# Kernel tuning notes

Hardware: AMD Instinct MI355X
Metric: run time of the kernel (lower is better)

Reference implementation:

```python
import jax, jax.numpy as jnp
import numpy as np

# Config constants (from DeepSeekConfig / init_kwargs)
NUM_EXPERTS = 6
VAR_EXPERTS = 4
FIXED_EXPERTS = NUM_EXPERTS - VAR_EXPERTS  # 2
TOP_K = 2
D_MODEL = 1024
D_FF = 4 * D_MODEL
LN_EPS = 1e-5


def setup_inputs() -> dict:
    key = jax.random.key(0)
    ks = jax.random.split(key, 6)
    B, S = 2, 2048
    x = jax.random.normal(ks[0], (B, S, D_MODEL), dtype=jnp.float32)
    router_W = jax.random.normal(ks[1], (D_MODEL, VAR_EXPERTS), dtype=jnp.float32) * 0.02
    # stacked expert FFN params: (E, D, 4D) and (E, 4D, D)
    W1 = jax.random.normal(ks[2], (NUM_EXPERTS, D_MODEL, D_FF), dtype=jnp.float32) * 0.02
    b1 = jnp.zeros((NUM_EXPERTS, D_FF), dtype=jnp.float32)
    W2 = jax.random.normal(ks[3], (NUM_EXPERTS, D_FF, D_MODEL), dtype=jnp.float32) * 0.02
    b2 = jnp.zeros((NUM_EXPERTS, D_MODEL), dtype=jnp.float32)
    ln_gamma = jnp.ones((D_MODEL,), dtype=jnp.float32)
    ln_beta = jnp.zeros((D_MODEL,), dtype=jnp.float32)
    return {"x": x, "router_W": router_W, "W1": W1, "b1": b1, "W2": W2,
            "b2": b2, "ln_gamma": ln_gamma, "ln_beta": ln_beta}


def reference(x, router_W, W1, b1, W2, b2, ln_gamma, ln_beta):
    B, S, D = x.shape
    # router over the VARIABLE experts only
    router_logits = jnp.einsum('bsd,de->bse', x, router_W)          # (B,S,VAR)
    router_probs = jax.nn.softmax(router_logits, axis=-1)
    _, topk_idx = jax.lax.top_k(router_probs, TOP_K)                 # (B,S,K)
    adj_idx = topk_idx + FIXED_EXPERTS                               # global expert ids in [FIXED, NUM)

    # dense per-expert FFN on all tokens: experts[e](x) = gelu(x@W1[e]+b1[e]) @ W2[e] + b2[e]
    h = jnp.einsum('bsd,edf->ebsf', x, W1) + b1[:, None, None, :]    # (E,B,S,4D)
    h = jax.nn.gelu(h, approximate=False)                            # torch F.gelu default = exact
    all_out = jnp.einsum('ebsf,efd->ebsd', h, W2) + b2[:, None, None, :]  # (E,B,S,D)

    # fixed experts: all of experts[0:FIXED] applied to every token
    fixed_sum = all_out[:FIXED_EXPERTS].sum(axis=0)                  # (B,S,D)

    # variable experts: per-token gather of the top-k selected experts
    b_ix = jnp.arange(B)[:, None, None]
    s_ix = jnp.arange(S)[None, :, None]
    var = all_out[adj_idx, b_ix, s_ix, :]                            # (B,S,K,D)

    # cat along expert slot dim then mean == sum / (FIXED + K); topk probs unused (plain mean)
    combined = (fixed_sum + var.sum(axis=2)) / (FIXED_EXPERTS + TOP_K)

    # LayerNorm (biased variance, eps=1e-5)
    mu = combined.mean(axis=-1, keepdims=True)
    v = combined.var(axis=-1, keepdims=True)
    out = (combined - mu) / jnp.sqrt(v + LN_EPS) * ln_gamma + ln_beta
    return out, router_logits
```

## Files before the change

### kernel.cpp

```cpp
#include <hip/hip_runtime.h>
#include <cstdint>
#include <cstddef>

#define D_MODEL 1024
#define D_FF 4096
#define NTOK 4096
#define LN_EPS 1e-5f
#define SLAB_ROWS 17408

typedef __bf16 bf16x8 __attribute__((ext_vector_type(8)));
typedef float f32x4 __attribute__((ext_vector_type(4)));
typedef unsigned short u16x4 __attribute__((ext_vector_type(4)));
typedef unsigned short u16x8 __attribute__((ext_vector_type(8)));

static __device__ __forceinline__ unsigned short f2bf(float f) {
    union { float f; unsigned u; } v; v.f = f;
    unsigned r = v.u + 0x7fffu + ((v.u >> 16) & 1u);
    return (unsigned short)(r >> 16);
}

static __device__ __forceinline__ float b2f(unsigned short u) {
    union { unsigned u; float f; } v; v.u = (unsigned)u << 16;
    return v.f;
}

static __device__ __forceinline__ float gelu_fast(float x) {
    float x2 = x * x;
    float a = x * __builtin_fmaf(-0.0713548162726f, x2, -1.59576912161f);
    float e = __expf(a);
    return x * __builtin_amdgcn_rcpf(1.0f + e);
}

static __device__ __forceinline__ void gload16(const void* g, void* l) {
    __builtin_amdgcn_global_load_lds(
        (const __attribute__((address_space(1))) void*)g,
        (__attribute__((address_space(3))) void*)l, 16, 0, 0);
}

static __device__ __forceinline__ void seg_of(const int* cnt, int seg[4], int pc[4]) {
    int o = 2 * NTOK;
    #pragma unroll
    for (int e = 0; e < 4; ++e) {
        int c = cnt[e * 32];
        pc[e] = (c + 255) & ~255;
        seg[e] = o;
        o += pc[e];
    }
}

__global__ __launch_bounds__(256) void convx_kernel(const float* __restrict__ x,
                                                    unsigned short* __restrict__ xb) {
    int idx = blockIdx.x * 256 + threadIdx.x;
    f32x4 v = *(const f32x4*)&x[(size_t)idx * 4];
    u16x4 b;
    b[0] = f2bf(v[0]); b[1] = f2bf(v[1]); b[2] = f2bf(v[2]); b[3] = f2bf(v[3]);
    *(u16x4*)&xb[(size_t)idx * 4] = b;
}

__global__ __launch_bounds__(256) void transpose_kernel(const float* __restrict__ W,
                                                        unsigned short* __restrict__ Wt,
                                                        int K, int N) {
    __shared__ unsigned short t[64][65];
    int k0 = blockIdx.y * 64, n0 = blockIdx.x * 64;
    const float* We = W + (size_t)blockIdx.z * K * N;
    unsigned short* Wte = Wt + (size_t)blockIdx.z * K * N;
    #pragma unroll
    for (int i = 0; i < 4; ++i) {
        int idx = threadIdx.x + i * 256;
        int kr = idx >> 4, c4 = idx & 15;
        f32x4 v = *(const f32x4*)&We[(size_t)(k0 + kr) * N + n0 + c4 * 4];
        #pragma unroll
        for (int j = 0; j < 4; ++j) t[c4 * 4 + j][kr] = f2bf(v[j]);
    }
    __syncthreads();
    #pragma unroll
    for (int i = 0; i < 2; ++i) {
        int idx = threadIdx.x + i * 256;
        int nr = idx >> 3, ck = idx & 7;
        u16x8 w;
        #pragma unroll
        for (int j = 0; j < 8; ++j) w[j] = t[nr][ck * 8 + j];
        *(u16x8*)&Wte[(size_t)(n0 + nr) * K + k0 + ck * 8] = w;
    }
}

__global__ __launch_bounds__(256) void router_kernel(
        const float* __restrict__ x, const float* __restrict__ rW,
        float* __restrict__ logits, int* __restrict__ selpk,
        int* __restrict__ slotpk, int* __restrict__ cnt, int* __restrict__ list) {
    __shared__ int se[8];
    __shared__ int sslot[8];
    int wid = threadIdx.x >> 6, lane = threadIdx.x & 63;
    int t = blockIdx.x * 4 + wid;
    const float* xr = x + (size_t)t * D_MODEL;
    float a0 = 0.f, a1 = 0.f, a2 = 0.f, a3 = 0.f;
    for (int d = lane; d < D_MODEL; d += 64) {
        float xv = xr[d];
        const float* w = rW + d * 4;
        a0 += xv * w[0]; a1 += xv * w[1]; a2 += xv * w[2]; a3 += xv * w[3];
    }
    #pragma unroll
    for (int off = 32; off; off >>= 1) {
        a0 += __shfl_xor(a0, off); a1 += __shfl_xor(a1, off);
        a2 += __shfl_xor(a2, off); a3 += __shfl_xor(a3, off);
    }
    if (lane == 0) {
        float l[4] = {a0, a1, a2, a3};
        logits[t * 4 + 0] = a0; logits[t * 4 + 1] = a1;
        logits[t * 4 + 2] = a2; logits[t * 4 + 3] = a3;
        int e0 = 0; float b = l[0];
        #pragma unroll
        for (int e = 1; e < 4; ++e) if (l[e] > b) { b = l[e]; e0 = e; }
        int e1 = -1; float b2 = -1e30f;
        #pragma unroll
        for (int e = 0; e < 4; ++e) {
            if (e == e0) continue;
            if (l[e] > b2) { b2 = l[e]; e1 = e; }
        }
        se[wid * 2] = e0; se[wid * 2 + 1] = e1;
    }
    __syncthreads();
    if (threadIdx.x == 0) {
        int cnts[4] = {0, 0, 0, 0}, base[4];
        #pragma unroll
        for (int k = 0; k < 8; ++k) cnts[se[k]]++;
        #pragma unroll
        for (int e = 0; e < 4; ++e)
            if (cnts[e]) base[e] = atomicAdd(&cnt[e * 32], cnts[e]);
        int run[4] = {0, 0, 0, 0};
        #pragma unroll
        for (int k = 0; k < 8; ++k) {
            int e = se[k];
            int s = base[e] + run[e]++;
            sslot[k] = s;
            list[e * NTOK + s] = blockIdx.x * 4 + (k >> 1);
        }
    }
    __syncthreads();
    if (lane == 0) {
        selpk[t] = se[wid * 2] | (se[wid * 2 + 1] << 8);
        slotpk[t] = sslot[wid * 2] | (sslot[wid * 2 + 1] << 16);
    }
}

template<int GELU>
__global__ __launch_bounds__(512, 2) void gemm8_kernel(
        const unsigned short* __restrict__ A, const unsigned short* __restrict__ B,
        const float* __restrict__ bias, int bias_stride, int ldo,
        unsigned short* __restrict__ out,
        const int* __restrict__ cnt, const int* __restrict__ list, int K) {
    __shared__ unsigned short lds[2][2][256 * 64];
    const int e = blockIdx.z;
    const int tid = threadIdx.x, l = tid & 63, w = tid >> 6;
    int rowbase;
    int ecnt = NTOK;
    if (e < 2) {
        rowbase = e * NTOK + blockIdx.y * 256;
    } else {
        int seg[4], pc[4];
        seg_of(cnt, seg, pc);
        int ev = e - 2;
        ecnt = cnt[ev * 32];
        if ((int)blockIdx.y * 256 >= pc[ev]) return;
        rowbase = seg[ev] + blockIdx.y * 256;
    }
    const int n0 = blockIdx.x * 256;
    const unsigned short* Be = B + (size_t)e * (4096 * 1024);

    const unsigned short* asrc[4];
    const unsigned short* bsrc[4];
    #pragma unroll
    for (int i = 0; i < 4; ++i) {
        int row = i * 64 + w * 8 + (l >> 3);
        int piece = ((l & 7) ^ (row & 7)) << 3;
        size_t arow;
        if (GELU) {
            int s = blockIdx.y * 256 + row;
            if (e < 2) arow = (size_t)s;
            else       arow = (size_t)((s < ecnt) ? list[(e - 2) * NTOK + s] : 0);
        } else {
            arow = (size_t)(rowbase + row);
        }
        asrc[i] = A + arow * K + piece;
        bsrc[i] = Be + (size_t)(n0 + row) * K + piece;
    }

    const int wr = w >> 2, wc = w & 3;
    const int rl = l & 15, kq = l >> 4;

    float bv[4];
    #pragma unroll
    for (int ni = 0; ni < 4; ++ni)
        bv[ni] = bias[(size_t)e * bias_stride + n0 + wc * 64 + ni * 16 + rl];

    f32x4 acc[8][4];
    #pragma unroll
    for (int i = 0; i < 8; ++i)
        #pragma unroll
        for (int j = 0; j < 4; ++j) acc[i][j] = (f32x4)0.f;

    const int nt = K / 64;

    #define STAGE(bf, t)                                                        \
        {                                                                       \
            unsigned short* la = &lds[bf][0][(w * 8) * 64];                     \
            unsigned short* lb = &lds[bf][1][(w * 8) * 64];                     \
            _Pragma("unroll")                                                   \
            for (int i = 0; i < 4; ++i) {                                       \
                gload16(asrc[i] + (t) * 64, la + i * 4096);                     \
                gload16(bsrc[i] + (t) * 64, lb + i * 4096);                     \
            }                                                                   \
        }

    STAGE(0, 0);
    STAGE(1, 1);

    for (int t = 0; t < nt; ++t) {
        const int cur = t & 1;
        if (t < nt - 1) { asm volatile("s_waitcnt vmcnt(8)" ::: "memory"); }
        else            { asm volatile("s_waitcnt vmcnt(0)" ::: "memory"); }
        __builtin_amdgcn_s_barrier();
        const unsigned short* LA = &lds[cur][0][0];
        const unsigned short* LB = &lds[cur][1][0];
        #pragma unroll
        for (int kk = 0; kk < 2; ++kk) {
            bf16x8 bfr[4];
            #pragma unroll
            for (int ni = 0; ni < 4; ++ni) {
                int n = wc * 64 + ni * 16 + rl;
                bfr[ni] = *(const bf16x8*)&LB[n * 64 + (((kk * 4 + kq) ^ (n & 7)) << 3)];
            }
            #pragma unroll
            for (int mh = 0; mh < 2; ++mh) {
                bf16x8 afr[4];
                #pragma unroll
                for (int i = 0; i < 4; ++i) {
                    int r = wr * 128 + (mh * 4 + i) * 16 + rl;
                    afr[i] = *(const bf16x8*)&LA[r * 64 + (((kk * 4 + kq) ^ (r & 7)) << 3)];
                }
                __builtin_amdgcn_s_barrier();
                __builtin_amdgcn_s_setprio(1);
                #pragma unroll
                for (int i = 0; i < 4; ++i)
                    #pragma unroll
                    for (int ni = 0; ni < 4; ++ni)
                        acc[mh * 4 + i][ni] = __builtin_amdgcn_mfma_f32_16x16x32_bf16(
                            afr[i], bfr[ni], acc[mh * 4 + i][ni], 0, 0, 0);
                __builtin_amdgcn_s_setprio(0);
                __builtin_amdgcn_s_barrier();
            }
        }
        if (t + 2 < nt) STAGE(cur, t + 2);
    }
    #undef STAGE

    #pragma unroll
    for (int ni = 0; ni < 4; ++ni) {
        int c = n0 + wc * 64 + ni * 16 + rl;
        #pragma unroll
        for (int mi = 0; mi < 8; ++mi) {
            #pragma unroll
            for (int j = 0; j < 4; ++j) {
                int r = wr * 128 + mi * 16 + kq * 4 + j;
                float v = acc[mi][ni][j] + bv[ni];
                if (GELU) v = gelu_fast(v);
                out[(size_t)(rowbase + r) * ldo + c] = f2bf(v);
            }
        }
    }
}

__global__ __launch_bounds__(256) void pass3_kernel(
        const unsigned short* __restrict__ oslab, const int* __restrict__ selpk,
        const int* __restrict__ slotpk, const int* __restrict__ cnt,
        const float* __restrict__ gamma, const float* __restrict__ beta,
        float* __restrict__ out) {
    int t = blockIdx.x;
    int seg[4], pc[4];
    seg_of(cnt, seg, pc);
    int sp = selpk[t], sl = slotpk[t];
    int e0 = sp & 0xff, e1 = (sp >> 8) & 0xff;
    int s0 = sl & 0xffff, s1 = (sl >> 16) & 0xffff;
    const unsigned short* p0 = oslab + (size_t)t * D_MODEL;
    const unsigned short* p1 = oslab + (size_t)(NTOK + t) * D_MODEL;
    const unsigned short* p2 = oslab + (size_t)(seg[e0] + s0) * D_MODEL;
    const unsigned short* p3 = oslab + (size_t)(seg[e1] + s1) * D_MODEL;
    float c[4];
    float sum = 0.f, sq = 0.f;
    #pragma unroll
    for (int i = 0; i < 4; ++i) {
        int d = threadIdx.x + i * 256;
        float v = (b2f(p0[d]) + b2f(p1[d]) + b2f(p2[d]) + b2f(p3[d])) * 0.25f;
        c[i] = v; sum += v; sq += v * v;
    }
    #pragma unroll
    for (int off = 32; off; off >>= 1) {
        sum += __shfl_xor(sum, off);
        sq  += __shfl_xor(sq, off);
    }
    __shared__ float red[8];
    int lane = threadIdx.x & 63, wid = threadIdx.x >> 6;
    if (lane == 0) { red[wid] = sum; red[4 + wid] = sq; }
    __syncthreads();
    sum = red[0] + red[1] + red[2] + red[3];
    sq  = red[4] + red[5] + red[6] + red[7];
    float mean = sum * (1.0f / 1024.0f);
    float var = sq * (1.0f / 1024.0f) - mean * mean;
    float inv = rsqrtf(var + LN_EPS);
    #pragma unroll
    for (int i = 0; i < 4; ++i) {
        int d = threadIdx.x + i * 256;
        out[(size_t)t * D_MODEL + d] = (c[i] - mean) * inv * gamma[d] + beta[d];
    }
}

extern "C" void kernel_launch(void* const* d_in, const int* in_sizes, int n_in,
                              void* d_out, int out_size, void* d_ws, size_t ws_size,
                              hipStream_t stream) {
    const float* x   = (const float*)d_in[0];
    const float* rW  = (const float*)d_in[1];
    const float* W1  = (const float*)d_in[2];
    const float* b1  = (const float*)d_in[3];
    const float* W2  = (const float*)d_in[4];
    const float* b2  = (const float*)d_in[5];
    const float* gam = (const float*)d_in[6];
    const float* bet = (const float*)d_in[7];
    float* out = (float*)d_out;
    float* logits = out + (size_t)NTOK * D_MODEL;

    char* ws = (char*)d_ws;
    int* cnt    = (int*)ws;
    int* selpk  = (int*)(ws + 0x1000);
    int* slotpk = (int*)(ws + 0x6000);
    int* list   = (int*)(ws + 0xB000);
    unsigned short* xb    = (unsigned short*)(ws + 0x20000);
    unsigned short* W1t   = (unsigned short*)(ws + 0x820000);
    unsigned short* W2t   = (unsigned short*)(ws + 0x3820000);
    unsigned short* oslab = (unsigned short*)(ws + 0x6820000);
    unsigned short* h     = (unsigned short*)(ws + 0x8A20000);

    convx_kernel<<<NTOK * D_MODEL / 4 / 256, 256, 0, stream>>>(x, xb);
    transpose_kernel<<<dim3(D_FF / 64, D_MODEL / 64, 6), 256, 0, stream>>>(W1, W1t, D_MODEL, D_FF);
    transpose_kernel<<<dim3(D_MODEL / 64, D_FF / 64, 6), 256, 0, stream>>>(W2, W2t, D_FF, D_MODEL);
    hipMemsetAsync(cnt, 0, 512, stream);
    router_kernel<<<NTOK / 4, 256, 0, stream>>>(x, rW, logits, selpk, slotpk, cnt, list);

    gemm8_kernel<1><<<dim3(D_FF / 256, 16, 6), 512, 0, stream>>>(
        xb, W1t, b1, D_FF, D_FF, h, cnt, list, D_MODEL);
    gemm8_kernel<0><<<dim3(D_MODEL / 256, 16, 6), 512, 0, stream>>>(
        h, W2t, b2, D_MODEL, D_MODEL, oslab, cnt, list, D_FF);

    pass3_kernel<<<NTOK, 256, 0, stream>>>(oslab, selpk, slotpk, cnt, gam, bet, out);
}
```

Baseline: 548.2 us.

## Split GEMM LDS tiles into k-halves and interleave global loads with MFMA phases

Rearranges the shared-memory tile into two 32-wide k-half sub-buffers per stage, with a new XOR swizzle on 16-byte chunks. The main loop becomes four phases per k-tile. Each phase issues a slice of the next tiles' global loads, then waits and runs 16 MFMAs, so memory traffic is spread across the compute instead of arriving as one burst per tile. The aim is to hide global-load latency and smooth LDS and VMEM pressure. In exchange, the vmcnt wait bookkeeping gets intricate and easy to get wrong.

```diff
diff --git a/kernel.cpp b/kernel.cpp
--- a/kernel.cpp
+++ b/kernel.cpp
@@ -149,7 +149,7 @@
         const float* __restrict__ bias, int bias_stride, int ldo,
         unsigned short* __restrict__ out,
         const int* __restrict__ cnt, const int* __restrict__ list, int K) {
-    __shared__ unsigned short lds[2][2][256 * 64];
+    __shared__ unsigned short lds[2][2][2][256 * 32];
     const int e = blockIdx.z;
     const int tid = threadIdx.x, l = tid & 63, w = tid >> 6;
     int rowbase;
@@ -165,28 +165,30 @@
         rowbase = seg[ev] + blockIdx.y * 256;
     }
     const int n0 = blockIdx.x * 256;
-    const unsigned short* Be = B + (size_t)e * (4096 * 1024);
-
-    const unsigned short* asrc[4];
-    const unsigned short* bsrc[4];
-    #pragma unroll
-    for (int i = 0; i < 4; ++i) {
-        int row = i * 64 + w * 8 + (l >> 3);
-        int piece = ((l & 7) ^ (row & 7)) << 3;
+    const unsigned short* Be = B + (size_t)e * (D_FF * D_MODEL);
+
+    const char* sa[2];
+    const char* sb[2];
+    #pragma unroll
+    for (int j = 0; j < 2; ++j) {
+        int r = j * 128 + w * 16 + (l >> 2);
+        int c = ((l & 3) ^ (r & 3)) << 4;
         size_t arow;
         if (GELU) {
-            int s = blockIdx.y * 256 + row;
+            int s = blockIdx.y * 256 + r;
             if (e < 2) arow = (size_t)s;
             else       arow = (size_t)((s < ecnt) ? list[(e - 2) * NTOK + s] : 0);
         } else {
-            arow = (size_t)(rowbase + row);
-        }
-        asrc[i] = A + arow * K + piece;
-        bsrc[i] = Be + (size_t)(n0 + row) * K + piece;
+            arow = (size_t)(rowbase + r);
+        }
+        sa[j] = (const char*)(A + arow * K) + c;
+        sb[j] = (const char*)(Be + (size_t)(n0 + r) * K) + c;
     }
 
     const int wr = w >> 2, wc = w & 3;
     const int rl = l & 15, kq = l >> 4;
+    const int aoff = (wr * 128 + rl) * 64 + ((kq ^ (rl & 3)) << 4);
+    const int boff = (wc * 64 + rl) * 64 + ((kq ^ (rl & 3)) << 4);
 
     float bv[4];
     #pragma unroll
@@ -201,58 +203,63 @@
 
     const int nt = K / 64;
 
-    #define STAGE(bf, t)                                                        \
+    #define ISSUE(ut, kh, j)                                                    \
+        do {                                                                    \
+            int bi_ = (ut) & 1;                                                 \
+            gload16(sa[j] + (size_t)(ut) * 128 + (kh) * 64,                     \
+                    &lds[bi_][0][kh][(j * 8 + w) * 512]);                       \
+            gload16(sb[j] + (size_t)(ut) * 128 + (kh) * 64,                     \
+                    &lds[bi_][1][kh][(j * 8 + w) * 512]);                       \
+        } while (0)
+
+    #define PHASE(bf, kk, mh, STAGE, ENDVM)                                     \
         {                                                                       \
-            unsigned short* la = &lds[bf][0][(w * 8) * 64];                     \
-            unsigned short* lb = &lds[bf][1][(w * 8) * 64];                     \
+            const char* LA = (const char*)&lds[bf][0][kk][0];                   \
+            const char* LB = (const char*)&lds[bf][1][kk][0];                   \
+            bf16x8 afr[4], bfr[4];                                              \
             _Pragma("unroll")                                                   \
-            for (int i = 0; i < 4; ++i) {                                       \
-                gload16(asrc[i] + (t) * 64, la + i * 4096);                     \
-                gload16(bsrc[i] + (t) * 64, lb + i * 4096);                     \
-            }                                                                   \
-        }
-
-    STAGE(0, 0);
-    STAGE(1, 1);
+            for (int i_ = 0; i_ < 4; ++i_)                                      \
+                afr[i_] = *(const bf16x8*)(LA + aoff + (mh) * 4096 + i_ * 1024);\
+            _Pragma("unroll")                                                   \
+            for (int i_ = 0; i_ < 4; ++i_)                                      \
+                bfr[i_] = *(const bf16x8*)(LB + boff + i_ * 1024);              \
+            STAGE;                                                              \
+            __builtin_amdgcn_s_barrier();                                       \
+            asm volatile("s_waitcnt lgkmcnt(0)" ::: "memory");                  \
+            __builtin_amdgcn_sched_barrier(0);                                  \
+            __builtin_amdgcn_s_setprio(1);                                      \
+            _Pragma("unroll")                                                   \
+            for (int i_ = 0; i_ < 4; ++i_)                                      \
+                _Pragma("unroll")                                               \
+                for (int n_ = 0; n_ < 4; ++n_)                                  \
+                    acc[(mh) * 4 + i_][n_] =                                    \
+                        __builtin_amdgcn_mfma_f32_16x16x32_bf16(                \
+                            afr[i_], bfr[n_], acc[(mh) * 4 + i_][n_], 0, 0, 0); \
+            __builtin_amdgcn_s_setprio(0);                                      \
+            ENDVM;                                                              \
+            __builtin_amdgcn_s_barrier();                                       \
+        }
+
+    ISSUE(0, 0, 0); ISSUE(0, 0, 1);
+    ISSUE(0, 1, 0); ISSUE(0, 1, 1);
+    ISSUE(1, 0, 0); ISSUE(1, 0, 1);
+    asm volatile("s_waitcnt vmcnt(8)" ::: "memory");
+    __builtin_amdgcn_s_barrier();
 
     for (int t = 0; t < nt; ++t) {
-        const int cur = t & 1;
-        if (t < nt - 1) { asm volatile("s_waitcnt vmcnt(8)" ::: "memory"); }
-        else            { asm volatile("s_waitcnt vmcnt(0)" ::: "memory"); }
-        __builtin_amdgcn_s_barrier();
-        const unsigned short* LA = &lds[cur][0][0];
-        const unsigned short* LB = &lds[cur][1][0];
-        #pragma unroll
-        for (int kk = 0; kk < 2; ++kk) {
-            bf16x8 bfr[4];
-            #pragma unroll
-            for (int ni = 0; ni < 4; ++ni) {
-                int n = wc * 64 + ni * 16 + rl;
-                bfr[ni] = *(const bf16x8*)&LB[n * 64 + (((kk * 4 + kq) ^ (n & 7)) << 3)];
-            }
-            #pragma unroll
-            for (int mh = 0; mh < 2; ++mh) {
-                bf16x8 afr[4];
-                #pragma unroll
-                for (int i = 0; i < 4; ++i) {
-                    int r = wr * 128 + (mh * 4 + i) * 16 + rl;
-                    afr[i] = *(const bf16x8*)&LA[r * 64 + (((kk * 4 + kq) ^ (r & 7)) << 3)];
-                }
-                __builtin_amdgcn_s_barrier();
-                __builtin_amdgcn_s_setprio(1);
-                #pragma unroll
-                for (int i = 0; i < 4; ++i)
-                    #pragma unroll
-                    for (int ni = 0; ni < 4; ++ni)
-                        acc[mh * 4 + i][ni] = __builtin_amdgcn_mfma_f32_16x16x32_bf16(
-                            afr[i], bfr[ni], acc[mh * 4 + i][ni], 0, 0, 0);
-                __builtin_amdgcn_s_setprio(0);
-                __builtin_amdgcn_s_barrier();
-            }
-        }
-        if (t + 2 < nt) STAGE(cur, t + 2);
-    }
-    #undef STAGE
+        const int bf = t & 1;
+        PHASE(bf, 0, 0, { if (t + 1 < nt) ISSUE(t + 1, 1, 0); }, {});
+        PHASE(bf, 0, 1, { if (t + 1 < nt) ISSUE(t + 1, 1, 1); },
+              { if (t < nt - 1) { asm volatile("s_waitcnt vmcnt(8)" ::: "memory"); }
+                else            { asm volatile("s_waitcnt vmcnt(0)" ::: "memory"); } });
+        PHASE(bf, 1, 0, { if (t + 2 < nt) ISSUE(t + 2, 0, 0); }, {});
+        PHASE(bf, 1, 1, { if (t + 2 < nt) ISSUE(t + 2, 0, 1); },
+              { if (t < nt - 1) {
+                    if (t + 2 < nt) { asm volatile("s_waitcnt vmcnt(8)" ::: "memory"); }
+                    else            { asm volatile("s_waitcnt vmcnt(4)" ::: "memory"); } } });
+    }
+    #undef PHASE
+    #undef ISSUE
 
     #pragma unroll
     for (int ni = 0; ni < 4; ++ni) {
```

Measured after the change: 594.3 us. 1.08x slower.

## Use 128x256 GEMM tiles with triple-buffered LDS and fewer barriers

Applied to the files above, without the earlier changes.

The expert FFN GEMM moves from 256x256 tiles with a double-buffered LDS pipeline to 128x256 tiles with a three-stage ring buffer. The next tile's load is issued right after the single barrier per K-step, and the two extra barriers inside the MFMA loop are removed. Grid height doubles, which gives more blocks for load balance across the variable-size expert segments. In exchange, each block reuses less data from every B tile, and occupancy drops to one block per CU under the new launch bounds.

```diff
diff --git a/kernel.cpp b/kernel.cpp
--- a/kernel.cpp
+++ b/kernel.cpp
@@ -6,7 +6,6 @@
 #define D_FF 4096
 #define NTOK 4096
 #define LN_EPS 1e-5f
-#define SLAB_ROWS 17408
 
 typedef __bf16 bf16x8 __attribute__((ext_vector_type(8)));
 typedef float f32x4 __attribute__((ext_vector_type(4)));
@@ -144,127 +143,126 @@
 }
 
 template<int GELU>
-__global__ __launch_bounds__(512, 2) void gemm8_kernel(
+__global__ __launch_bounds__(512, 1) void gemm3r_kernel(
         const unsigned short* __restrict__ A, const unsigned short* __restrict__ B,
         const float* __restrict__ bias, int bias_stride, int ldo,
         unsigned short* __restrict__ out,
         const int* __restrict__ cnt, const int* __restrict__ list, int K) {
-    __shared__ unsigned short lds[2][2][256 * 64];
+    __shared__ unsigned short Al[3][128 * 64];
+    __shared__ unsigned short Bl[3][256 * 64];
     const int e = blockIdx.z;
     const int tid = threadIdx.x, l = tid & 63, w = tid >> 6;
     int rowbase;
     int ecnt = NTOK;
     if (e < 2) {
-        rowbase = e * NTOK + blockIdx.y * 256;
+        rowbase = e * NTOK + blockIdx.y * 128;
     } else {
         int seg[4], pc[4];
         seg_of(cnt, seg, pc);
         int ev = e - 2;
         ecnt = cnt[ev * 32];
-        if ((int)blockIdx.y * 256 >= pc[ev]) return;
-        rowbase = seg[ev] + blockIdx.y * 256;
+        if ((int)blockIdx.y * 128 >= pc[ev]) return;
+        rowbase = seg[ev] + blockIdx.y * 128;
     }
     const int n0 = blockIdx.x * 256;
-    const unsigned short* Be = B + (size_t)e * (4096 * 1024);
-
-    const unsigned short* asrc[4];
-    const unsigned short* bsrc[4];
-    #pragma unroll
-    for (int i = 0; i < 4; ++i) {
-        int row = i * 64 + w * 8 + (l >> 3);
-        int piece = ((l & 7) ^ (row & 7)) << 3;
+    const unsigned short* Be = B + (size_t)e * (D_FF * D_MODEL);
+
+    const unsigned short* sa[2];
+    const unsigned short* sb[4];
+    #pragma unroll
+    for (int i = 0; i < 2; ++i) {
+        int r = i * 64 + w * 8 + (l >> 3);
+        int piece = ((l & 7) ^ (r & 7)) << 3;
         size_t arow;
         if (GELU) {
-            int s = blockIdx.y * 256 + row;
+            int s = blockIdx.y * 128 + r;
             if (e < 2) arow = (size_t)s;
             else       arow = (size_t)((s < ecnt) ? list[(e - 2) * NTOK + s] : 0);
         } else {
-            arow = (size_t)(rowbase + row);
-        }
-        asrc[i] = A + arow * K + piece;
-        bsrc[i] = Be + (size_t)(n0 + row) * K + piece;
+            arow = (size_t)(rowbase + r);
+        }
+        sa[i] = A + arow * K + piece;
+    }
+    #pragma unroll
+    for (int i = 0; i < 4; ++i) {
+        int r = i * 64 + w * 8 + (l >> 3);
+        int piece = ((l & 7) ^ (r & 7)) << 3;
+        sb[i] = Be + (size_t)(n0 + r) * K + piece;
     }
 
     const int wr = w >> 2, wc = w & 3;
     const int rl = l & 15, kq = l >> 4;
 
-    float bv[4];
-    #pragma unroll
-    for (int ni = 0; ni < 4; ++ni)
-        bv[ni] = bias[(size_t)e * bias_stride + n0 + wc * 64 + ni * 16 + rl];
-
-    f32x4 acc[8][4];
-    #pragma unroll
-    for (int i = 0; i < 8; ++i)
+    f32x4 acc[4][4];
+    #pragma unroll
+    for (int i = 0; i < 4; ++i)
         #pragma unroll
         for (int j = 0; j < 4; ++j) acc[i][j] = (f32x4)0.f;
 
     const int nt = K / 64;
 
-    #define STAGE(bf, t)                                                        \
+    #define ISSUE(t)                                                            \
         {                                                                       \
-            unsigned short* la = &lds[bf][0][(w * 8) * 64];                     \
-            unsigned short* lb = &lds[bf][1][(w * 8) * 64];                     \
+            int bi_ = (t) % 3;                                                  \
+            unsigned short* la = &Al[bi_][(w * 8) * 64];                        \
+            unsigned short* lb = &Bl[bi_][(w * 8) * 64];                        \
             _Pragma("unroll")                                                   \
-            for (int i = 0; i < 4; ++i) {                                       \
-                gload16(asrc[i] + (t) * 64, la + i * 4096);                     \
-                gload16(bsrc[i] + (t) * 64, lb + i * 4096);                     \
-            }                                                                   \
-        }
-
-    STAGE(0, 0);
-    STAGE(1, 1);
+            for (int i_ = 0; i_ < 2; ++i_)                                      \
+                gload16(sa[i_] + (size_t)(t) * 64, la + i_ * 4096);             \
+            _Pragma("unroll")                                                   \
+            for (int i_ = 0; i_ < 4; ++i_)                                      \
+                gload16(sb[i_] + (size_t)(t) * 64, lb + i_ * 4096);             \
+        }
+
+    ISSUE(0);
+    ISSUE(1);
 
     for (int t = 0; t < nt; ++t) {
-        const int cur = t & 1;
-        if (t < nt - 1) { asm volatile("s_waitcnt vmcnt(8)" ::: "memory"); }
+        if (t + 1 < nt) { asm volatile("s_waitcnt vmcnt(6)" ::: "memory"); }
         else            { asm volatile("s_waitcnt vmcnt(0)" ::: "memory"); }
         __builtin_amdgcn_s_barrier();
-        const unsigned short* LA = &lds[cur][0][0];
-        const unsigned short* LB = &lds[cur][1][0];
+        if (t + 2 < nt) ISSUE(t + 2);
+        const unsigned short* LA = &Al[t % 3][0];
+        const unsigned short* LB = &Bl[t % 3][0];
         #pragma unroll
         for (int kk = 0; kk < 2; ++kk) {
-            bf16x8 bfr[4];
+            int kof = kk * 32 + kq * 8;
+            bf16x8 a[4], b[4];
+            #pragma unroll
+            for (int mi = 0; mi < 4; ++mi) {
+                int r = wr * 64 + mi * 16 + rl;
+                a[mi] = *(const bf16x8*)&LA[r * 64 + (kof ^ ((r & 7) << 3))];
+            }
             #pragma unroll
             for (int ni = 0; ni < 4; ++ni) {
                 int n = wc * 64 + ni * 16 + rl;
-                bfr[ni] = *(const bf16x8*)&LB[n * 64 + (((kk * 4 + kq) ^ (n & 7)) << 3)];
+                b[ni] = *(const bf16x8*)&LB[n * 64 + (kof ^ ((n & 7) << 3))];
             }
+            __builtin_amdgcn_s_setprio(1);
             #pragma unroll
-            for (int mh = 0; mh < 2; ++mh) {
-                bf16x8 afr[4];
+            for (int mi = 0; mi < 4; ++mi)
                 #pragma unroll
-                for (int i = 0; i < 4; ++i) {
-                    int r = wr * 128 + (mh * 4 + i) * 16 + rl;
-                    afr[i] = *(const bf16x8*)&LA[r * 64 + (((kk * 4 + kq) ^ (r & 7)) << 3)];
-                }
-                __builtin_amdgcn_s_barrier();
-                __builtin_amdgcn_s_setprio(1);
-                #pragma unroll
-                for (int i = 0; i < 4; ++i)
-                    #pragma unroll
-                    for (int ni = 0; ni < 4; ++ni)
-                        acc[mh * 4 + i][ni] = __builtin_amdgcn_mfma_f32_16x16x32_bf16(
-                            afr[i], bfr[ni], acc[mh * 4 + i][ni], 0, 0, 0);
-                __builtin_amdgcn_s_setprio(0);
-                __builtin_amdgcn_s_barrier();
-            }
-        }
-        if (t + 2 < nt) STAGE(cur, t + 2);
-    }
-    #undef STAGE
-
+                for (int ni = 0; ni < 4; ++ni)
+                    acc[mi][ni] = __builtin_amdgcn_mfma_f32_16x16x32_bf16(
+                        a[mi], b[ni], acc[mi][ni], 0, 0, 0);
+            __builtin_amdgcn_s_setprio(0);
+        }
+    }
+    #undef ISSUE
+
+    const float* be = bias + (size_t)e * bias_stride + n0;
     #pragma unroll
     for (int ni = 0; ni < 4; ++ni) {
-        int c = n0 + wc * 64 + ni * 16 + rl;
-        #pragma unroll
-        for (int mi = 0; mi < 8; ++mi) {
+        int cc = wc * 64 + ni * 16 + rl;
+        float bv = be[cc];
+        #pragma unroll
+        for (int mi = 0; mi < 4; ++mi) {
             #pragma unroll
             for (int j = 0; j < 4; ++j) {
-                int r = wr * 128 + mi * 16 + kq * 4 + j;
-                float v = acc[mi][ni][j] + bv[ni];
+                int r = wr * 64 + mi * 16 + kq * 4 + j;
+                float v = acc[mi][ni][j] + bv;
                 if (GELU) v = gelu_fast(v);
-                out[(size_t)(rowbase + r) * ldo + c] = f2bf(v);
+                out[(size_t)(rowbase + r) * ldo + n0 + cc] = f2bf(v);
             }
         }
     }
@@ -345,9 +343,9 @@
     hipMemsetAsync(cnt, 0, 512, stream);
     router_kernel<<<NTOK / 4, 256, 0, stream>>>(x, rW, logits, selpk, slotpk, cnt, list);
 
-    gemm8_kernel<1><<<dim3(D_FF / 256, 16, 6), 512, 0, stream>>>(
+    gemm3r_kernel<1><<<dim3(D_FF / 256, 32, 6), 512, 0, stream>>>(
         xb, W1t, b1, D_FF, D_FF, h, cnt, list, D_MODEL);
-    gemm8_kernel<0><<<dim3(D_MODEL / 256, 16, 6), 512, 0, stream>>>(
+    gemm3r_kernel<0><<<dim3(D_MODEL / 256, 32, 6), 512, 0, stream>>>(
         h, W2t, b2, D_MODEL, D_MODEL, oslab, cnt, list, D_FF);
 
     pass3_kernel<<<NTOK, 256, 0, stream>>>(oslab, selpk, slotpk, cnt, gam, bet, out);
```

Measured after the change: 672.9 us. 22.8% more time.
